# Kernel tuning notes

Hardware: AMD Instinct MI355X
Metric: run time of the kernel (lower is better)

Reference implementation:

```python
import jax, jax.numpy as jnp
import numpy as np

N_NODES = 65536
IN_DIM = 256
HIDDEN = 256
NUM_GRAPHS = 128   # B = batch.max()+1; fixed by construction in setup_inputs
MAX_LEN = 1024     # >= max per-graph length (avg 512, binomial tail << 1024)


def _uniform(key, shape, scale):
    return jax.random.uniform(key, shape, jnp.float32, -scale, scale)


def setup_inputs() -> dict:
    key = jax.random.key(0)
    ks = jax.random.split(key, 12)
    x = jax.random.normal(ks[0], (N_NODES, IN_DIM), jnp.float32)
    batch = jnp.sort(jax.random.randint(ks[1], (N_NODES,), 0, NUM_GRAPHS)).astype(jnp.int64)
    s = 1.0 / np.sqrt(HIDDEN)  # torch nn.GRU init: U(-1/sqrt(H), 1/sqrt(H))
    # gate order follows torch: (r, z, n) stacked along first axis -> 3H rows
    params = {
        'W_ih0': _uniform(ks[2], (3 * HIDDEN, IN_DIM), s),
        'W_hh0': _uniform(ks[3], (3 * HIDDEN, HIDDEN), s),
        'b_ih0': _uniform(ks[4], (3 * HIDDEN,), s),
        'b_hh0': _uniform(ks[5], (3 * HIDDEN,), s),
        'W_ih1': _uniform(ks[6], (3 * HIDDEN, HIDDEN), s),
        'W_hh1': _uniform(ks[7], (3 * HIDDEN, HIDDEN), s),
        'b_ih1': _uniform(ks[8], (3 * HIDDEN,), s),
        'b_hh1': _uniform(ks[9], (3 * HIDDEN,), s),
    }
    return {'x': x, 'batch': batch, **params}


def _gru_layer(xs, W_ih, W_hh, b_ih, b_hh):
    # xs: [B, L, D] -> [B, L, H]; torch GRU cell math, gate order (r, z, n)
    B = xs.shape[0]
    H = W_hh.shape[1]
    gx = jnp.einsum('bld,gd->blg', xs, W_ih) + b_ih  # precompute input gates, one big GEMM

    def step(h, gx_t):
        gh = h @ W_hh.T + b_hh
        xr, xz, xn = jnp.split(gx_t, 3, axis=-1)
        hr, hz, hn = jnp.split(gh, 3, axis=-1)
        r = jax.nn.sigmoid(xr + hr)
        z = jax.nn.sigmoid(xz + hz)
        n = jnp.tanh(xn + r * hn)
        h_new = (1.0 - z) * n + z * h
        return h_new, h_new

    h0 = jnp.zeros((B, H), xs.dtype)
    _, hs = jax.lax.scan(step, h0, jnp.swapaxes(gx, 0, 1))  # [L, B, H]
    return jnp.swapaxes(hs, 0, 1)


def reference(x, batch, W_ih0, W_hh0, b_ih0, b_hh0, W_ih1, W_hh1, b_ih1, b_hh1):
    # Ragged per-graph sequences -> padded [B, MAX_LEN, D]. Padding is at the
    # end of each row; GRU is causal so valid positions match the per-graph
    # loop in the original module exactly, and the masked mean ignores padding.
    N, D = x.shape
    b32 = batch.astype(jnp.int32)
    counts = jax.ops.segment_sum(jnp.ones((N,), jnp.float32), b32, num_segments=NUM_GRAPHS)
    starts = jnp.cumsum(counts) - counts              # exclusive prefix sum
    pos = jnp.arange(N, dtype=jnp.float32) - starts[b32]
    pos = pos.astype(jnp.int32)                       # position within graph

    xp = jnp.zeros((NUM_GRAPHS, MAX_LEN, D), x.dtype).at[b32, pos].set(x)
    mask = jnp.zeros((NUM_GRAPHS, MAX_LEN), x.dtype).at[b32, pos].set(1.0)

    h = _gru_layer(xp, W_ih0, W_hh0, b_ih0, b_hh0)
    h = _gru_layer(h, W_ih1, W_hh1, b_ih1, b_hh1)

    denom = jnp.maximum(counts, 1.0)[:, None]
    out = jnp.sum(h * mask[:, :, None], axis=1) / denom  # mean over valid steps
    return out  # dropout is identity at eval
```

## Files before the change

kernel.cpp:

```cpp
#include <hip/hip_runtime.h>
#include <hip/hip_bf16.h>

typedef _Float16 half2_t __attribute__((ext_vector_type(2)));
typedef _Float16 f16x8   __attribute__((ext_vector_type(8)));
typedef float    f32x4   __attribute__((ext_vector_type(4)));
typedef unsigned short u16;
typedef unsigned int   u32;

#define N_NODES 65536
#define IN_DIM  256
#define HIDDEN  256
#define G3      768
#define NGRAPH  128

__device__ __forceinline__ float sigf(float x)    { return 1.f / (1.f + __expf(-x)); }
__device__ __forceinline__ float tanhfast(float x){ return 2.f / (1.f + __expf(-2.f * x)) - 1.f; }

__global__ void k_starts(const int* __restrict__ batch, int* __restrict__ starts, int n, int ngraph) {
    int g = blockIdx.x * blockDim.x + threadIdx.x;
    if (g > ngraph) return;
    int stride = (batch[n - 1] == 0) ? 2 : 1;
    if (g == ngraph) { starts[g] = n; return; }
    int lo = 0, hi = n;
    while (lo < hi) { int mid = (lo + hi) >> 1; if (batch[(size_t)mid * stride] < g) lo = mid + 1; else hi = mid; }
    starts[g] = lo;
}

__global__ void k_cvt8(const float* __restrict__ s, u16* __restrict__ d, int n) {
    int t = blockIdx.x * 256 + threadIdx.x;
    int i = t * 8;
    if (i >= n) return;
    float4 a = ((const float4*)(s + i))[0];
    float4 b = ((const float4*)(s + i))[1];
    f16x8 o;
    o[0] = (_Float16)a.x; o[1] = (_Float16)a.y; o[2] = (_Float16)a.z; o[3] = (_Float16)a.w;
    o[4] = (_Float16)b.x; o[5] = (_Float16)b.y; o[6] = (_Float16)b.z; o[7] = (_Float16)b.w;
    *(f16x8*)(d + i) = o;
}

__global__ void k_swz(const float* __restrict__ W, uint4* __restrict__ out) {
    int t = blockIdx.x * 256 + threadIdx.x;
    if (t >= 24576) return;
    int l = t & 63, i = (t >> 6) & 15, rest = t >> 10;
    int w = rest / 3, rg = rest % 3;
    int row = rg * 256 + (w & 3) * 64 + l;
    int col = (w >> 2) * 128 + i * 8;
    const float* s = W + row * 256 + col;
    f16x8 o;
#pragma unroll
    for (int q = 0; q < 8; q++) o[q] = (_Float16)s[q];
    out[t] = __builtin_bit_cast(uint4, o);
}

template <typename AT>
__global__ __launch_bounds__(256) void k_gemm(
    const AT* __restrict__ A, const u16* __restrict__ Bm,
    const float* __restrict__ bias, u16* __restrict__ C,
    int M, int N, int K)
{
    __shared__ u16 As[128 * 40];
    __shared__ u16 Bs[128 * 40];
    const int m0 = blockIdx.y * 128, n0 = blockIdx.x * 128;
    const int t = threadIdx.x;
    const int wave = t >> 6, lane = t & 63;
    const int wm = wave & 1, wn = wave >> 1;
    const int lr = lane & 15, lq = lane >> 4;
    f32x4 acc[4][4] = {};
    const int sr = t >> 1, sp = t & 1;
    const AT*  gA = A  + (size_t)(m0 + sr) * K + sp * 16;
    const u16* gB = Bm + (size_t)(n0 + sr) * K + sp * 16;
    u16* sA = As + sr * 40 + sp * 16;
    u16* sB = Bs + sr * 40 + sp * 16;
    for (int kt = 0; kt < K; kt += 32) {
        uint4 av0, av1;
        if constexpr (sizeof(AT) == 4) {
            float4 a0 = ((const float4*)gA)[0], a1 = ((const float4*)gA)[1];
            float4 a2 = ((const float4*)gA)[2], a3 = ((const float4*)gA)[3];
            f16x8 lo, hi;
            lo[0]=(_Float16)a0.x; lo[1]=(_Float16)a0.y; lo[2]=(_Float16)a0.z; lo[3]=(_Float16)a0.w;
            lo[4]=(_Float16)a1.x; lo[5]=(_Float16)a1.y; lo[6]=(_Float16)a1.z; lo[7]=(_Float16)a1.w;
            hi[0]=(_Float16)a2.x; hi[1]=(_Float16)a2.y; hi[2]=(_Float16)a2.z; hi[3]=(_Float16)a2.w;
            hi[4]=(_Float16)a3.x; hi[5]=(_Float16)a3.y; hi[6]=(_Float16)a3.z; hi[7]=(_Float16)a3.w;
            av0 = __builtin_bit_cast(uint4, lo);
            av1 = __builtin_bit_cast(uint4, hi);
        } else {
            av0 = ((const uint4*)gA)[0];
            av1 = ((const uint4*)gA)[1];
        }
        uint4 b0 = ((const uint4*)gB)[0], b1 = ((const uint4*)gB)[1];
        gA += 32; gB += 32;
        __syncthreads();
        ((uint4*)sA)[0] = av0; ((uint4*)sA)[1] = av1;
        ((uint4*)sB)[0] = b0;  ((uint4*)sB)[1] = b1;
        __syncthreads();
        f16x8 af[4], bf[4];
#pragma unroll
        for (int i = 0; i < 4; i++)
            af[i] = *(const f16x8*)(As + (wm * 64 + i * 16 + lr) * 40 + lq * 8);
#pragma unroll
        for (int j = 0; j < 4; j++)
            bf[j] = *(const f16x8*)(Bs + (wn * 64 + j * 16 + lr) * 40 + lq * 8);
#pragma unroll
        for (int i = 0; i < 4; i++)
#pragma unroll
            for (int j = 0; j < 4; j++)
                acc[i][j] = __builtin_amdgcn_mfma_f32_16x16x32_f16(af[i], bf[j], acc[i][j], 0, 0, 0);
    }
#pragma unroll
    for (int i = 0; i < 4; i++) {
        int row = m0 + wm * 64 + i * 16 + lq * 4;
#pragma unroll
        for (int j = 0; j < 4; j++) {
            int col = n0 + wn * 64 + j * 16 + lr;
            float bv = bias[col];
#pragma unroll
            for (int rr = 0; rr < 4; rr++) {
                _Float16 v = (_Float16)(acc[i][j][rr] + bv);
                C[(size_t)(row + rr) * N + col] = __builtin_bit_cast(u16, v);
            }
        }
    }
}

__global__ __launch_bounds__(512, 2) void k_rec(
    const u16* __restrict__ gx,
    const uint4* __restrict__ wsw,
    const float* __restrict__ bhh,
    const int*   __restrict__ starts,
    u16* __restrict__ hout,
    float* __restrict__ out)
{
    __shared__ float part[4][HIDDEN];
    __shared__ uint4 hpk4[HIDDEN / 8];
    const int g = blockIdx.x;
    const int tid = threadIdx.x;
    const int h = tid & 255;
    const int kh = tid >> 8;
    const int wv = tid >> 6, l = tid & 63;
    const int start = starts[g];
    const int len = starts[g + 1] - start;
    uint4 w[3][16];
#pragma unroll
    for (int rg = 0; rg < 3; rg++)
#pragma unroll
        for (int i = 0; i < 16; i++)
            w[rg][i] = wsw[(size_t)(((wv * 3 + rg) * 16 + i) * 64 + l)];
#pragma unroll
    for (int rg = 0; rg < 3; rg++)
#pragma unroll
        for (int i = 0; i < 16; i++)
            asm volatile("" : "+v"(w[rg][i].x), "+v"(w[rg][i].y), "+v"(w[rg][i].z), "+v"(w[rg][i].w));
    const float bhr = bhh[h], bhz = bhh[h + 256], bhn = bhh[h + 512];
    if (tid < HIDDEN / 8) hpk4[tid] = make_uint4(0, 0, 0, 0);
    float hp = 0.f, hs = 0.f;
    const _Float16* gxr = (const _Float16*)gx + (size_t)start * G3 + h;
    u16* hrow = hout ? (hout + (size_t)start * HIDDEN + h) : (u16*)nullptr;
    float gr = 0.f, gz = 0.f, gn = 0.f;
    if (kh && len > 0) { gr = (float)gxr[0]; gz = (float)gxr[256]; gn = (float)gxr[512]; }
    __syncthreads();
    for (int t = 0; t < len; ++t) {
        float pr = 0.f, pz = 0.f, pn = 0.f;
        if (kh) {
            int tn = t + 1 < len ? t + 1 : len - 1;
            size_t o1 = (size_t)tn * G3;
            pr = (float)gxr[o1]; pz = (float)gxr[o1 + 256]; pn = (float)gxr[o1 + 512];
        }
        float ar0 = kh ? gr : bhr, ar1 = 0.f;
        float az0 = kh ? gz : bhz, az1 = 0.f;
        float an0 = kh ? 0.f : bhn, an1 = 0.f;
#pragma unroll
        for (int i = 0; i < 16; i++) {
            uint4 hv = hpk4[kh * 16 + i];
            half2_t hx = __builtin_bit_cast(half2_t, hv.x), hy = __builtin_bit_cast(half2_t, hv.y);
            half2_t hz2 = __builtin_bit_cast(half2_t, hv.z), hw = __builtin_bit_cast(half2_t, hv.w);
            ar0 = __builtin_amdgcn_fdot2(__builtin_bit_cast(half2_t, w[0][i].x), hx, ar0, false);
            ar1 = __builtin_amdgcn_fdot2(__builtin_bit_cast(half2_t, w[0][i].y), hy, ar1, false);
            ar0 = __builtin_amdgcn_fdot2(__builtin_bit_cast(half2_t, w[0][i].z), hz2, ar0, false);
            ar1 = __builtin_amdgcn_fdot2(__builtin_bit_cast(half2_t, w[0][i].w), hw, ar1, false);
            az0 = __builtin_amdgcn_fdot2(__builtin_bit_cast(half2_t, w[1][i].x), hx, az0, false);
            az1 = __builtin_amdgcn_fdot2(__builtin_bit_cast(half2_t, w[1][i].y), hy, az1, false);
            az0 = __builtin_amdgcn_fdot2(__builtin_bit_cast(half2_t, w[1][i].z), hz2, az0, false);
            az1 = __builtin_amdgcn_fdot2(__builtin_bit_cast(half2_t, w[1][i].w), hw, az1, false);
            an0 = __builtin_amdgcn_fdot2(__builtin_bit_cast(half2_t, w[2][i].x), hx, an0, false);
            an1 = __builtin_amdgcn_fdot2(__builtin_bit_cast(half2_t, w[2][i].y), hy, an1, false);
            an0 = __builtin_amdgcn_fdot2(__builtin_bit_cast(half2_t, w[2][i].z), hz2, an0, false);
            an1 = __builtin_amdgcn_fdot2(__builtin_bit_cast(half2_t, w[2][i].w), hw, an1, false);
        }
        float sr = ar0 + ar1, sz = az0 + az1, sn = an0 + an1;
        if (kh) { part[0][h] = sr; part[1][h] = sz; part[2][h] = sn; part[3][h] = gn; }
        __syncthreads();
        if (!kh) {
            float r = sigf(sr + part[0][h]);
            float z = sigf(sz + part[1][h]);
            float n = tanhfast(part[3][h] + r * (sn + part[2][h]));
            float hnew = (1.f - z) * n + z * hp;
            hp = hnew; hs += hnew;
            _Float16 ph = (_Float16)hnew;
            u16 pk = __builtin_bit_cast(u16, ph);
            ((u16*)hpk4)[h] = pk;
            if (hrow) hrow[(size_t)t * HIDDEN] = pk;
        }
        gr = pr; gz = pz; gn = pn;
        __syncthreads();
    }
    if (out && !kh) {
        float inv = 1.f / (float)(len > 0 ? len : 1);
        out[g * HIDDEN + h] = hs * inv;
    }
}

extern "C" void kernel_launch(void* const* d_in, const int* in_sizes, int n_in,
                              void* d_out, int out_size, void* d_ws, size_t ws_size,
                              hipStream_t stream)
{
    const float* x     = (const float*)d_in[0];
    const int*   batch = (const int*)d_in[1];
    const float* Wih0  = (const float*)d_in[2];
    const float* Whh0  = (const float*)d_in[3];
    const float* bih0  = (const float*)d_in[4];
    const float* bhh0  = (const float*)d_in[5];
    const float* Wih1  = (const float*)d_in[6];
    const float* Whh1  = (const float*)d_in[7];
    const float* bih1  = (const float*)d_in[8];
    const float* bhh1  = (const float*)d_in[9];
    float* out = (float*)d_out;

    char* ws = (char*)d_ws;
    size_t o = 0;
    int*   starts = (int*)  (ws + o); o += 4096;
    u16*   wi0    = (u16*)  (ws + o); o += (size_t)G3 * IN_DIM * 2;
    u16*   wi1    = (u16*)  (ws + o); o += (size_t)G3 * HIDDEN * 2;
    uint4* wsw0   = (uint4*)(ws + o); o += (size_t)G3 * HIDDEN * 2;
    uint4* wsw1   = (uint4*)(ws + o); o += (size_t)G3 * HIDDEN * 2;
    u16*   h0     = (u16*)  (ws + o); o += (size_t)N_NODES * HIDDEN * 2;
    u16*   gxbuf  = (u16*)  (ws + o); o += (size_t)N_NODES * G3 * 2;

    k_starts<<<1, 256, 0, stream>>>(batch, starts, N_NODES, NGRAPH);
    k_cvt8<<<96, 256, 0, stream>>>(Wih0, wi0, G3 * IN_DIM);
    k_cvt8<<<96, 256, 0, stream>>>(Wih1, wi1, G3 * HIDDEN);
    k_swz<<<96, 256, 0, stream>>>(Whh0, wsw0);
    k_swz<<<96, 256, 0, stream>>>(Whh1, wsw1);

    k_gemm<float><<<dim3(G3 / 128, N_NODES / 128), 256, 0, stream>>>(x, wi0, bih0, gxbuf, N_NODES, G3, IN_DIM);
    k_rec<<<NGRAPH, 512, 0, stream>>>(gxbuf, wsw0, bhh0, starts, h0, (float*)nullptr);
    k_gemm<_Float16><<<dim3(G3 / 128, N_NODES / 128), 256, 0, stream>>>((const _Float16*)h0, wi1, bih1, gxbuf, N_NODES, G3, HIDDEN);
    k_rec<<<NGRAPH, 512, 0, stream>>>(gxbuf, wsw1, bhh1, starts, (u16*)nullptr, out);
}
```

Baseline: 1.795 ms.

## Split GRU recurrent matvec K-dimension across four thread quarters

The recurrent kernel now runs 1024 threads per graph instead of 512, and splits the hidden-state dot product into four K-quarters instead of two. Each thread holds half as many swizzled weight registers, and the weight swizzle layout is changed to match. The h_hh bias moves into one slice of shared memory so the owner quarter can sum four partials with the input gates. This is meant to shorten the serial per-timestep dot-product latency. The costs are a larger block barrier, extra shared-memory reduction reads, and a possible register cap from the new launch bounds.

```diff
diff --git a/kernel.cpp b/kernel.cpp
--- a/kernel.cpp
+++ b/kernel.cpp
@@ -41,10 +41,10 @@
 __global__ void k_swz(const float* __restrict__ W, uint4* __restrict__ out) {
     int t = blockIdx.x * 256 + threadIdx.x;
     if (t >= 24576) return;
-    int l = t & 63, i = (t >> 6) & 15, rest = t >> 10;
-    int w = rest / 3, rg = rest % 3;
-    int row = rg * 256 + (w & 3) * 64 + l;
-    int col = (w >> 2) * 128 + i * 8;
+    int l = t & 63, i = (t >> 6) & 7, rest = t >> 9;
+    int wv = rest / 3, rg = rest % 3;
+    int row = rg * 256 + (wv & 3) * 64 + l;
+    int col = (wv >> 2) * 64 + i * 8;
     const float* s = W + row * 256 + col;
     f16x8 o;
 #pragma unroll
@@ -122,7 +122,7 @@
     }
 }
 
-__global__ __launch_bounds__(512, 2) void k_rec(
+__global__ __launch_bounds__(1024, 4) void k_rec(
     const u16* __restrict__ gx,
     const uint4* __restrict__ wsw,
     const float* __restrict__ bhh,
@@ -130,80 +130,76 @@
     u16* __restrict__ hout,
     float* __restrict__ out)
 {
-    __shared__ float part[4][HIDDEN];
+    __shared__ float part[3][4][HIDDEN];
     __shared__ uint4 hpk4[HIDDEN / 8];
     const int g = blockIdx.x;
     const int tid = threadIdx.x;
     const int h = tid & 255;
-    const int kh = tid >> 8;
+    const int q = tid >> 8;
     const int wv = tid >> 6, l = tid & 63;
     const int start = starts[g];
     const int len = starts[g + 1] - start;
-    uint4 w[3][16];
+    uint4 w[3][8];
 #pragma unroll
     for (int rg = 0; rg < 3; rg++)
 #pragma unroll
-        for (int i = 0; i < 16; i++)
-            w[rg][i] = wsw[(size_t)(((wv * 3 + rg) * 16 + i) * 64 + l)];
-#pragma unroll
-    for (int rg = 0; rg < 3; rg++)
-#pragma unroll
-        for (int i = 0; i < 16; i++)
-            asm volatile("" : "+v"(w[rg][i].x), "+v"(w[rg][i].y), "+v"(w[rg][i].z), "+v"(w[rg][i].w));
-    const float bhr = bhh[h], bhz = bhh[h + 256], bhn = bhh[h + 512];
+        for (int i = 0; i < 8; i++)
+            w[rg][i] = wsw[(size_t)(((wv * 3 + rg) * 8 + i) * 64 + l)];
+    if (tid < G3) part[tid >> 8][0][tid & 255] = bhh[tid];
     if (tid < HIDDEN / 8) hpk4[tid] = make_uint4(0, 0, 0, 0);
     float hp = 0.f, hs = 0.f;
     const _Float16* gxr = (const _Float16*)gx + (size_t)start * G3 + h;
     u16* hrow = hout ? (hout + (size_t)start * HIDDEN + h) : (u16*)nullptr;
     float gr = 0.f, gz = 0.f, gn = 0.f;
-    if (kh && len > 0) { gr = (float)gxr[0]; gz = (float)gxr[256]; gn = (float)gxr[512]; }
+    if (q == 0 && len > 0) { gr = (float)gxr[0]; gz = (float)gxr[256]; gn = (float)gxr[512]; }
+    const int qb = q * 8;
     __syncthreads();
     for (int t = 0; t < len; ++t) {
         float pr = 0.f, pz = 0.f, pn = 0.f;
-        if (kh) {
+        if (q == 0) {
             int tn = t + 1 < len ? t + 1 : len - 1;
             size_t o1 = (size_t)tn * G3;
             pr = (float)gxr[o1]; pz = (float)gxr[o1 + 256]; pn = (float)gxr[o1 + 512];
         }
-        float ar0 = kh ? gr : bhr, ar1 = 0.f;
-        float az0 = kh ? gz : bhz, az1 = 0.f;
-        float an0 = kh ? 0.f : bhn, an1 = 0.f;
-#pragma unroll
-        for (int i = 0; i < 16; i++) {
-            uint4 hv = hpk4[kh * 16 + i];
+        float ar = 0.f, az = 0.f, an = 0.f;
+#pragma unroll
+        for (int i = 0; i < 8; i++) {
+            uint4 hv = hpk4[qb + i];
             half2_t hx = __builtin_bit_cast(half2_t, hv.x), hy = __builtin_bit_cast(half2_t, hv.y);
             half2_t hz2 = __builtin_bit_cast(half2_t, hv.z), hw = __builtin_bit_cast(half2_t, hv.w);
-            ar0 = __builtin_amdgcn_fdot2(__builtin_bit_cast(half2_t, w[0][i].x), hx, ar0, false);
-            ar1 = __builtin_amdgcn_fdot2(__builtin_bit_cast(half2_t, w[0][i].y), hy, ar1, false);
-            ar0 = __builtin_amdgcn_fdot2(__builtin_bit_cast(half2_t, w[0][i].z), hz2, ar0, false);
-            ar1 = __builtin_amdgcn_fdot2(__builtin_bit_cast(half2_t, w[0][i].w), hw, ar1, false);
-            az0 = __builtin_amdgcn_fdot2(__builtin_bit_cast(half2_t, w[1][i].x), hx, az0, false);
-            az1 = __builtin_amdgcn_fdot2(__builtin_bit_cast(half2_t, w[1][i].y), hy, az1, false);
-            az0 = __builtin_amdgcn_fdot2(__builtin_bit_cast(half2_t, w[1][i].z), hz2, az0, false);
-            az1 = __builtin_amdgcn_fdot2(__builtin_bit_cast(half2_t, w[1][i].w), hw, az1, false);
-            an0 = __builtin_amdgcn_fdot2(__builtin_bit_cast(half2_t, w[2][i].x), hx, an0, false);
-            an1 = __builtin_amdgcn_fdot2(__builtin_bit_cast(half2_t, w[2][i].y), hy, an1, false);
-            an0 = __builtin_amdgcn_fdot2(__builtin_bit_cast(half2_t, w[2][i].z), hz2, an0, false);
-            an1 = __builtin_amdgcn_fdot2(__builtin_bit_cast(half2_t, w[2][i].w), hw, an1, false);
-        }
-        float sr = ar0 + ar1, sz = az0 + az1, sn = an0 + an1;
-        if (kh) { part[0][h] = sr; part[1][h] = sz; part[2][h] = sn; part[3][h] = gn; }
-        __syncthreads();
-        if (!kh) {
-            float r = sigf(sr + part[0][h]);
-            float z = sigf(sz + part[1][h]);
-            float n = tanhfast(part[3][h] + r * (sn + part[2][h]));
+            ar = __builtin_amdgcn_fdot2(__builtin_bit_cast(half2_t, w[0][i].x), hx, ar, false);
+            az = __builtin_amdgcn_fdot2(__builtin_bit_cast(half2_t, w[1][i].x), hx, az, false);
+            an = __builtin_amdgcn_fdot2(__builtin_bit_cast(half2_t, w[2][i].x), hx, an, false);
+            ar = __builtin_amdgcn_fdot2(__builtin_bit_cast(half2_t, w[0][i].y), hy, ar, false);
+            az = __builtin_amdgcn_fdot2(__builtin_bit_cast(half2_t, w[1][i].y), hy, az, false);
+            an = __builtin_amdgcn_fdot2(__builtin_bit_cast(half2_t, w[2][i].y), hy, an, false);
+            ar = __builtin_amdgcn_fdot2(__builtin_bit_cast(half2_t, w[0][i].z), hz2, ar, false);
+            az = __builtin_amdgcn_fdot2(__builtin_bit_cast(half2_t, w[1][i].z), hz2, az, false);
+            an = __builtin_amdgcn_fdot2(__builtin_bit_cast(half2_t, w[2][i].z), hz2, an, false);
+            ar = __builtin_amdgcn_fdot2(__builtin_bit_cast(half2_t, w[0][i].w), hw, ar, false);
+            az = __builtin_amdgcn_fdot2(__builtin_bit_cast(half2_t, w[1][i].w), hw, az, false);
+            an = __builtin_amdgcn_fdot2(__builtin_bit_cast(half2_t, w[2][i].w), hw, an, false);
+        }
+        if (q) { part[0][q][h] = ar; part[1][q][h] = az; part[2][q][h] = an; }
+        __syncthreads();
+        if (!q) {
+            float sr = ar + part[0][0][h] + part[0][1][h] + part[0][2][h] + part[0][3][h];
+            float sz = az + part[1][0][h] + part[1][1][h] + part[1][2][h] + part[1][3][h];
+            float sn = an + part[2][0][h] + part[2][1][h] + part[2][2][h] + part[2][3][h];
+            float r = sigf(gr + sr);
+            float z = sigf(gz + sz);
+            float n = tanhfast(gn + r * sn);
             float hnew = (1.f - z) * n + z * hp;
             hp = hnew; hs += hnew;
             _Float16 ph = (_Float16)hnew;
             u16 pk = __builtin_bit_cast(u16, ph);
             ((u16*)hpk4)[h] = pk;
             if (hrow) hrow[(size_t)t * HIDDEN] = pk;
-        }
-        gr = pr; gz = pz; gn = pn;
-        __syncthreads();
-    }
-    if (out && !kh) {
+            gr = pr; gz = pz; gn = pn;
+        }
+        __syncthreads();
+    }
+    if (out && !q) {
         float inv = 1.f / (float)(len > 0 ? len : 1);
         out[g * HIDDEN + h] = hs * inv;
     }
@@ -242,7 +238,7 @@
     k_swz<<<96, 256, 0, stream>>>(Whh1, wsw1);
 
     k_gemm<float><<<dim3(G3 / 128, N_NODES / 128), 256, 0, stream>>>(x, wi0, bih0, gxbuf, N_NODES, G3, IN_DIM);
-    k_rec<<<NGRAPH, 512, 0, stream>>>(gxbuf, wsw0, bhh0, starts, h0, (float*)nullptr);
+    k_rec<<<NGRAPH, 1024, 0, stream>>>(gxbuf, wsw0, bhh0, starts, h0, (float*)nullptr);
     k_gemm<_Float16><<<dim3(G3 / 128, N_NODES / 128), 256, 0, stream>>>((const _Float16*)h0, wi1, bih1, gxbuf, N_NODES, G3, HIDDEN);
-    k_rec<<<NGRAPH, 512, 0, stream>>>(gxbuf, wsw1, bhh1, starts, (u16*)nullptr, out);
-}
+    k_rec<<<NGRAPH, 1024, 0, stream>>>(gxbuf, wsw1, bhh1, starts, (u16*)nullptr, out);
+}
```

After: 1.549 ms. -13.7%, faster.
